# Performance work log

Hardware: AMD Instinct MI355X
Metric: run time of the kernel (lower is better)

## Reference

```python
import jax, jax.numpy as jnp
import numpy as np

B, C, H, W = 16, 1, 512, 512
D, F, KH, KW = 4, 24, 5, 5   # numWienerFilters, output_features, reg-filter size
BKH, BKW = 9, 9              # blur kernel size
LB, UB = 1e-4, 1e-2


def psf2otf(psf, shape):
    # zero-pad psf to `shape`, circularly shift its center to (0,0), FFT
    kh, kw = psf.shape[-2], psf.shape[-1]
    pad = [(0, 0)] * (psf.ndim - 2) + [(0, shape[0] - kh), (0, shape[1] - kw)]
    p = jnp.pad(psf, pad)
    p = jnp.roll(p, shift=(-((kh - 1) // 2), -((kw - 1) // 2)), axis=(-2, -1))
    return jnp.fft.fft2(p)


def _taper_profile(proj, n):
    # autocorrelation of the psf projection, periodized to length n (MATLAB edgetaper)
    z = jnp.zeros(n - 1, proj.dtype).at[: proj.shape[0]].set(proj)
    zf = jnp.fft.fft(z)
    acf = jnp.real(jnp.fft.ifft(zf * jnp.conj(zf)))
    acf = jnp.concatenate([acf, acf[:1]])
    return acf / acf.max()


def _normalize_weights(w, scale):
    # WeightNormalization5D: zero-mean + L2-normalize over (C,kh,kw), times scale
    w = w - w.mean(axis=(2, 3, 4), keepdims=True)
    nrm = jnp.sqrt(jnp.sum(w * w, axis=(2, 3, 4), keepdims=True))
    return w * (scale[..., None, None, None] / nrm)


def setup_inputs():
    key = jax.random.key(0)
    ks = jax.random.split(key, 4)
    x = jax.random.uniform(ks[0], (B, C, H, W), jnp.float32)
    bk = jax.random.uniform(ks[1], (BKH, BKW), jnp.float32) + 1e-3
    bk = bk / bk.sum()  # normalized blur PSF
    stdn = jax.random.uniform(ks[2], (B,), jnp.float32) * 0.1 + 0.01
    conv_weights = jax.random.normal(ks[3], (D, F, C, KH, KW), jnp.float32)
    scale = jnp.full((D, F), 0.1, jnp.float32)
    alpha = jnp.log(jnp.logspace(np.log10(LB), np.log10(UB), D))[:, None].astype(jnp.float32)
    return {"x": x, "blur_kernel": bk, "stdn": stdn,
            "conv_weights": conv_weights, "scale": scale, "alpha": alpha}


def reference(x, blur_kernel, stdn, conv_weights, scale, alpha):
    kh, kw = blur_kernel.shape
    # getPad2RetainShape
    pt, pb = (kh + 1) // 2 - 1, kh - (kh + 1) // 2
    pl, pr = (kw + 1) // 2 - 1, kw - (kw + 1) // 2
    xp = jnp.pad(x, ((0, 0), (0, 0), (pt, pb), (pl, pr)), mode="symmetric")
    Hp, Wp = xp.shape[-2], xp.shape[-1]
    otf = psf2otf(blur_kernel, (Hp, Wp))                     # (Hp,Wp) complex
    # EdgeTaper: blend image with its circular blur near borders
    br = _taper_profile(blur_kernel.sum(axis=1), Hp)
    bc = _taper_profile(blur_kernel.sum(axis=0), Wp)
    taper = (1.0 - br)[:, None] * (1.0 - bc)[None, :]
    blurred = jnp.real(jnp.fft.ifft2(jnp.fft.fft2(xp) * otf))
    xp = taper * xp + (1.0 - taper) * blurred
    # regularization-filter OTFs
    w = _normalize_weights(conv_weights, scale)              # (D,F,C,kh,kw)
    G = psf2otf(w, (Hp, Wp))                                 # (D,F,C,Hp,Wp)
    S = jnp.sum(G.real ** 2 + G.imag ** 2, axis=1)           # (D,C,Hp,Wp)
    a = jnp.exp(alpha)[:, :, None, None]                     # (D,1,1,1)
    B2 = otf.real ** 2 + otf.imag ** 2                       # (Hp,Wp)
    denom = B2[None, None] + a * S                           # (D,C,Hp,Wp)
    Y = jnp.conj(otf) * jnp.fft.fft2(xp)                     # (B,C,Hp,Wp)
    Xf = Y[:, None] / denom[None]                            # (B,D,C,Hp,Wp)
    out = jnp.real(jnp.fft.ifft2(Xf))[..., pt:Hp - pb, pl:Wp - pr]
    # colored-noise std factor per (wiener filter, channel)
    cvar = jnp.mean(B2[None, None] / denom ** 2, axis=(-2, -1))   # (D,C)
    cvar = jnp.broadcast_to(cvar[None], (x.shape[0],) + cvar.shape)  # (B,D,C)
    cstdn = jnp.sqrt(stdn[:, None] ** 2 * cvar.mean(axis=2))        # (B,D)
    return out, cstdn
```

## Files before the change

kernel.cpp:

```cpp
#include <hip/hip_runtime.h>
#include <math.h>

#define NP    520
#define NN    (520*520)
#define HH    512
#define NPIX  (512*512)
#define NB    16
#define NPAIR 8
#define ND    4
#define NF    24
#define KS    544
#define RS    576
#define PLANE ((size_t)RS*KS)
#define S8P   (8*PLANE)
#define E9SZ  (NP*9)
#define CSZ   (ND*9*NP)
#define NBORD 18396
#define PADCH 5536
#define NBLK2 1057
#define TWO_PI 6.283185307179586f

typedef unsigned short u16;
typedef __attribute__((ext_vector_type(8))) short bf16x8;
typedef __attribute__((ext_vector_type(4))) float f32x4;

__device__ __forceinline__ int wrap520(int t){ t %= NP; return t < 0 ? t + NP : t; }

__device__ __forceinline__ u16 f2bf(float f){
  unsigned u = __float_as_uint(f);
  u += 0x7FFFu + ((u >> 16) & 1u);
  return (u16)(u >> 16);
}
__device__ __forceinline__ float bf2f(u16 h){
  return __uint_as_float(((unsigned)h) << 16);
}
__device__ __forceinline__ void gll16(const u16* g, u16* l){
  __builtin_amdgcn_global_load_lds(
      (const __attribute__((address_space(1))) void*)g,
      (__attribute__((address_space(3))) void*)l, 16, 0, 0);
}
template<int N> __device__ __forceinline__ void vmwait(){
  if constexpr (N == 0)       asm volatile("s_waitcnt vmcnt(0)" ::: "memory");
  else if constexpr (N == 4)  asm volatile("s_waitcnt vmcnt(4)" ::: "memory");
  else if constexpr (N == 6)  asm volatile("s_waitcnt vmcnt(6)" ::: "memory");
  else if constexpr (N == 8)  asm volatile("s_waitcnt vmcnt(8)" ::: "memory");
  else if constexpr (N == 12) asm volatile("s_waitcnt vmcnt(12)" ::: "memory");
}
#define MF(a,b,c) __builtin_amdgcn_mfma_f32_16x16x32_bf16((a),(b),(c),0,0,0)


__global__ __launch_bounds__(256) void zwb_k(u16* __restrict__ slabs,
                                             u16* __restrict__ wf, u16* __restrict__ wi){
  int idx = blockIdx.x*256 + threadIdx.x;
  const int nA = 16*PADCH;
  if (idx < nA){
    int pl = idx / PADCH, cc = idx % PADCH;
    int row, col;
    if (cc < 1728){ row = cc/3; col = 520 + (cc%3)*8; }
    else { int c2 = cc - 1728; row = 520 + c2/68; col = (c2%68)*8; }
    bf16x8 z = {0,0,0,0,0,0,0,0};
    *(bf16x8*)(slabs + (size_t)pl*PLANE + (size_t)row*KS + col) = z;
    return;
  }
  idx -= nA;
  if (idx >= (int)PLANE) return;
  int r = idx / KS, k = idx % KS;
  float fr=0.f, fi=0.f, ir=0.f, ii=0.f;
  if (r < NP && k < NP){
    int m = (int)(((long long)r * (long long)k) % NP);
    float ang = TWO_PI * (float)m / (float)NP;
    float s, c; sincosf(ang, &s, &c);
    fr = c; fi = -s;
    ir = c * (1.0f/NP); ii = s * (1.0f/NP);
  }
  wf[0*PLANE+idx] = f2bf(fr); wf[1*PLANE+idx] = f2bf(fi);
  wi[0*PLANE+idx] = f2bf(ir); wi[1*PLANE+idx] = f2bf(ii);
}

__global__ __launch_bounds__(256) void setup1_k(const float* __restrict__ bk,
                                                const float* __restrict__ cw,
                                                const float* __restrict__ scale,
                                                float* __restrict__ e9,
                                                float* __restrict__ r_row, float* __restrict__ r_col,
                                                float* __restrict__ wn){
  int idx = blockIdx.x*256 + threadIdx.x;
  if (idx < NP*9){
    int u = idx / 9, t = idx % 9;
    int m = wrap520(u*(t-4));
    float ang = TWO_PI * (float)m / (float)NP;
    float s, c; sincosf(ang, &s, &c);
    e9[idx] = c; e9[E9SZ + idx] = -s;
    return;
  }
  idx -= NP*9;
  if (idx < 18){
    int k = idx % 9;
    bool rowp = (idx < 9);
    float proj[9];
    for (int m = 0; m < 9; ++m){
      float a = 0.f;
      for (int j = 0; j < 9; ++j) a += rowp ? bk[m*9+j] : bk[j*9+m];
      proj[m] = a;
    }
    float acc = 0.f;
    for (int m = 0; m + k < 9; ++m) acc += proj[m] * proj[m+k];
    (rowp ? r_row : r_col)[k] = acc;
    return;
  }
  idx -= 18;
  if (idx >= ND*NF) return;
  const float* wp = cw + idx*25;
  float mean = 0.f;
  for (int k = 0; k < 25; ++k) mean += wp[k];
  mean *= (1.0f/25.0f);
  float ss = 0.f;
  for (int k = 0; k < 25; ++k){ float d = wp[k]-mean; ss += d*d; }
  float sc = scale[idx] / sqrtf(ss);
  for (int k = 0; k < 25; ++k) wn[idx*25+k] = (wp[k]-mean)*sc;
}

__global__ __launch_bounds__(256) void setup2_k(const float* __restrict__ bk,
                                                const float* __restrict__ e9,
                                                const float* __restrict__ wn,
                                                float* __restrict__ T, float* __restrict__ R){
  int idx = blockIdx.x*256 + threadIdx.x;
  if (idx < 9*NP){
    int i = idx / NP, v = idx % NP;
    float tr = 0.f, ti = 0.f;
    #pragma unroll
    for (int j = 0; j < 9; ++j){
      float w = bk[i*9+j];
      tr += w * e9[v*9+j];
      ti += w * e9[E9SZ + v*9+j];
    }
    T[idx] = tr; T[9*NP + idx] = ti;
    return;
  }
  idx -= 9*NP;
  if (idx >= ND*81) return;
  int d = idx / 81, t = idx % 81;
  int di = t/9 - 4, dj = t%9 - 4;
  int i0 = di > 0 ? di : 0, i1 = di < 0 ? 4+di : 4;
  int j0 = dj > 0 ? dj : 0, j1 = dj < 0 ? 4+dj : 4;
  float acc = 0.f;
  for (int f = 0; f < NF; ++f){
    const float* w = wn + (d*NF+f)*25;
    for (int i = i0; i <= i1; ++i)
      for (int j = j0; j <= j1; ++j)
        acc += w[i*5+j] * w[(i-di)*5 + (j-dj)];
  }
  R[idx] = acc;
}

__global__ void C_k(const float* __restrict__ R, const float* __restrict__ e9,
                    float* __restrict__ Ctab){
  int idx = blockIdx.x*blockDim.x + threadIdx.x;
  if (idx >= ND*9*NP) return;
  int v = idx % NP, t9 = idx / NP;
  int d = t9 / 9, t = t9 % 9;
  float cr = 0.f, ci = 0.f;
  #pragma unroll
  for (int s = 0; s < 9; ++s){
    float r = R[d*81 + t*9 + s];
    cr += r * e9[v*9+s];
    ci += r * e9[E9SZ + v*9+s];
  }
  Ctab[idx] = cr; Ctab[CSZ + idx] = ci;
}

__global__ __launch_bounds__(256) void denomMT2_k(
    const float* __restrict__ Tb, const float* __restrict__ e9,
    const float* __restrict__ Ctab, const float* __restrict__ alpha,
    u16* __restrict__ MTre, u16* __restrict__ MTim, float* __restrict__ pcv){
  __shared__ float e9r[2304], e9i[2304];
  __shared__ float red[256];
  const int tid = threadIdx.x;
  const int p = blockIdx.x*256 + tid;
  {
    int u0 = (blockIdx.x*256) % NP;
    for (int i = tid; i < 2304; i += 256){
      int row = i / 9, col = i % 9;
      int uu = u0 + row; if (uu >= NP) uu -= NP;
      e9r[i] = e9[uu*9 + col];
      e9i[i] = e9[E9SZ + uu*9 + col];
    }
  }
  __syncthreads();
  float contrib[ND] = {0.f, 0.f, 0.f, 0.f};
  if (p < NN){
    int v = p / NP;
    float er9[9], ei9[9];
    #pragma unroll
    for (int i = 0; i < 9; ++i){ er9[i] = e9r[tid*9+i]; ei9[i] = e9i[tid*9+i]; }
    float ar = 0.f, ai = 0.f;
    #pragma unroll
    for (int i = 0; i < 9; ++i){
      float tr = Tb[i*NP+v], ti = Tb[9*NP + i*NP+v];
      ar += er9[i]*tr - ei9[i]*ti;
      ai += er9[i]*ti + ei9[i]*tr;
    }
    float B2 = ar*ar + ai*ai;
    #pragma unroll
    for (int d = 0; d < ND; ++d){
      float S = 0.f;
      #pragma unroll
      for (int t = 0; t < 9; ++t)
        S += er9[t]*Ctab[(d*9+t)*NP + v] - ei9[t]*Ctab[CSZ + (d*9+t)*NP + v];
      float dv = B2 + expf(alpha[d]) * S;
      MTre[(size_t)d*NN + p] = f2bf(ar / dv);
      MTim[(size_t)d*NN + p] = f2bf(-ai / dv);
      contrib[d] = B2 / (dv*dv);
    }
  }
  for (int d = 0; d < ND; ++d){
    red[tid] = contrib[d]; __syncthreads();
    for (int s = 128; s > 0; s >>= 1){
      if (tid < s) red[tid] += red[tid+s];
      __syncthreads();
    }
    if (tid == 0) pcv[(size_t)blockIdx.x*ND + d] = red[0];
    __syncthreads();
  }
}

__global__ __launch_bounds__(256) void cstdn2_k(const float* __restrict__ stdn,
                                                const float* __restrict__ pcv,
                                                float* __restrict__ out){
  __shared__ float red[256];
  int t = threadIdx.x;
  int d = t & 3, ch = t >> 2;
  float acc = 0.f;
  for (int b = ch; b < NBLK2; b += 64) acc += pcv[(size_t)b*ND + d];
  red[t] = acc; __syncthreads();
  for (int s = 128; s >= 4; s >>= 1){
    if (t < s) red[t] += red[t+s];
    __syncthreads();
  }
  if (t < NB*ND){
    int b = t >> 2, d2 = t & 3;
    float s = stdn[b];
    out[(size_t)NB*ND*NPIX + t] = sqrtf(s*s*red[d2]*(1.0f/(float)NN));
  }
}

__global__ __launch_bounds__(256) void pad_tr_k(const float* __restrict__ x,
                                                u16* __restrict__ MA){
  __shared__ float tile[64][65];
  const int q  = blockIdx.z;
  const int r0 = blockIdx.y * 64;
  const int c0 = blockIdx.x * 64;
  const int t  = threadIdx.x;
  const float* xq = x + (size_t)q*NPIX;
  const int jl = t & 63, ib = t >> 6;
  const bool fast = (c0 >= 64 && c0 <= 448 && r0 >= 64 && r0 <= 448);

  if (fast){
    #pragma unroll 1
    for (int pass = 0; pass < 16; ++pass){
      int il = ib + pass*4;
      tile[il][jl] = xq[(size_t)(c0+il-4)*HH + (r0+jl-4)];
    }
  } else {
    #pragma unroll 1
    for (int pass = 0; pass < 16; ++pass){
      int il = ib + pass*4;
      int I = c0 + il, J = r0 + jl;
      float v = 0.f;
      if (I < NP && J < NP){
        int si = I - 4; si = (si < 0) ? (-si-1) : ((si >= HH) ? (2*HH-1-si) : si);
        int sj = J - 4; sj = (sj < 0) ? (-sj-1) : ((sj >= HH) ? (2*HH-1-sj) : sj);
        v = xq[(size_t)si*HH + sj];
      }
      tile[il][jl] = v;
    }
  }
  __syncthreads();

  const int cchunk = t & 7, rb = t >> 3;
  const int pair = q >> 1, pl = q & 1;
  #pragma unroll
  for (int half = 0; half < 2; ++half){
    int rl = rb + half*32;
    int r = r0 + rl, cg = c0 + cchunk*8;
    if (r >= NP || cg >= NP) continue;
    bf16x8 vh;
    #pragma unroll
    for (int e = 0; e < 8; ++e)
      vh[e] = (short)f2bf(tile[cchunk*8+e][rl]);
    size_t o = (size_t)pair*PLANE + (size_t)r*KS + cg;
    *(bf16x8*)(MA + (size_t)pl*S8P + o) = vh;
  }
}

__global__ __launch_bounds__(256) void border_k(const float* __restrict__ x,
                                                const float* __restrict__ bk,
                                                const float* __restrict__ r_row,
                                                const float* __restrict__ r_col,
                                                u16* __restrict__ MA){
  __shared__ float bks[81], rr_[9], rc_[9];
  if (threadIdx.x < 81) bks[threadIdx.x] = bk[threadIdx.x];
  if (threadIdx.x < 9){ rr_[threadIdx.x] = r_row[threadIdx.x]; rc_[threadIdx.x] = r_col[threadIdx.x]; }
  __syncthreads();
  int idx = blockIdx.x*256 + threadIdx.x;
  if (idx >= NB*NBORD) return;
  int q = idx / NBORD, t = idx % NBORD;
  int I, J;
  if (t < 9360){ int ri = t / 520; I = (ri < 9) ? ri : 502 + ri; J = t % 520; }
  else { int s = t - 9360; I = 9 + s / 18; int ci = s % 18; J = (ci < 9) ? ci : 502 + ci; }
  const float* xq = x + (size_t)q*NPIX;
  auto XP = [&](int ii, int jj)->float{
    int si = ii - 4; si = (si < 0) ? (-si-1) : ((si >= HH) ? (2*HH-1-si) : si);
    int sj = jj - 4; sj = (sj < 0) ? (-sj-1) : ((sj >= HH) ? (2*HH-1-sj) : sj);
    return xq[(size_t)si*HH + sj];
  };
  float v = XP(I, J);
  float brv = (I < 9) ? rr_[I] : ((I >= 511) ? rr_[519-I] : 0.f);
  float bcv = (J < 9) ? rc_[J] : ((J >= 511) ? rc_[519-J] : 0.f);
  brv /= rr_[0]; bcv /= rc_[0];
  float tp = (1.f - brv) * (1.f - bcv);
  float blur = 0.f;
  for (int a = 0; a < 9; ++a){
    int ii = wrap520(I - a + 4);
    for (int b2 = 0; b2 < 9; ++b2){
      int jj = wrap520(J - b2 + 4);
      blur += bks[a*9+b2] * XP(ii, jj);
    }
  }
  v = tp*v + (1.f - tp)*blur;
  int pair = q >> 1, pl = q & 1;
  MA[(size_t)pl*S8P + (size_t)pair*PLANE + (size_t)J*KS + I] = f2bf(v);
}

__global__ __launch_bounds__(256) void maskF_k(const u16* __restrict__ IN, u16* __restrict__ OUT,
                                               const u16* __restrict__ Mre, const u16* __restrict__ Mim){
  int idx = blockIdx.x*256 + threadIdx.x;
  if (idx >= NPAIR*NP*65) return;
  int pr = idx / (NP*65), rem = idx % (NP*65);
  int r = rem / 65, c0 = (rem % 65)*8;
  size_t o = (size_t)pr*PLANE + (size_t)r*KS + c0;
  bf16x8 qr = *(const bf16x8*)(IN + 0*S8P + o);
  bf16x8 qi = *(const bf16x8*)(IN + 1*S8P + o);
  const u16* mrp = Mre + (size_t)r*NP + c0;
  const u16* mip = Mim + (size_t)r*NP + c0;
  bf16x8 o0, o1;
  #pragma unroll
  for (int e = 0; e < 8; ++e){
    float vr = bf2f((u16)qr[e]), vi = bf2f((u16)qi[e]);
    float mr = bf2f(mrp[e]), mi = bf2f(mip[e]);
    o0[e] = (short)f2bf(vr*mr - vi*mi);
    o1[e] = (short)f2bf(vr*mi + vi*mr);
  }
  *(bf16x8*)(OUT + 0*S8P + o) = o0;
  *(bf16x8*)(OUT + 1*S8P + o) = o1;
}

template<int BM, int CROP, int MASKOUT>
__global__ __launch_bounds__(256) void gemm_k(
    const u16* __restrict__ P, size_t pPl, size_t pZp, size_t pZd,
    const u16* __restrict__ Q, size_t qPl, size_t qZp, size_t qZd,
    u16* __restrict__ O, size_t oPl, size_t oZp, size_t oZd,
    float* __restrict__ cropOut, int dBase,
    const u16* __restrict__ Mre, const u16* __restrict__ Mim)
{
  constexpr int NW = 4;
  constexpr int FR = BM/32;
  constexpr int TR = BM/16;
  constexpr int LPW = 4*TR/NW;
  constexpr int PLSTR = BM*32;
  constexpr int BUF = 4*PLSTR;
  constexpr int NK = KS/32;
  __shared__ u16 lds[3*BUF];
  const int tid = threadIdx.x;
  const int l = tid & 63, w = tid >> 6;

  const int gx = gridDim.x, gy = gridDim.y;
  int lin = blockIdx.x + gx*(blockIdx.y + gy*blockIdx.z);
  int ntot = gx*gy*gridDim.z;
  int q8 = ntot >> 3, r8 = ntot & 7;
  int xcd = lin & 7, id8 = lin >> 3;
  int nl = (xcd < r8 ? xcd*(q8+1) : r8*(q8+1) + (xcd-r8)*q8) + id8;
  int BX = nl % gx; int t2 = nl / gx;
  int BY = t2 % gy; int BZ = t2 / gy;

  const int pair = BZ & 7;
  const int dd = dBase + (BZ >> 3);
  const int R0 = BY * BM, C0 = BX * BM;

  const u16* Pb = P + (size_t)pair*pZp + (size_t)dd*pZd;
  const u16* Qb = Q + (size_t)pair*qZp + (size_t)dd*qZd;

  const int s = l >> 2;
  const int cs8 = ((l & 3) ^ ((s >> 1) & 3)) * 8;
  const size_t pOff0 = (size_t)(R0 + s)*KS + cs8;
  const size_t qOff0 = (size_t)(C0 + s)*KS + cs8;

  const int lm = l & 15, lc = l >> 4;
  const int wm = w >> 1, wn = w & 1;

  f32x4 zero4 = {0.f, 0.f, 0.f, 0.f};
  f32x4 aRe[FR][FR], aIm[FR][FR];
  #pragma unroll
  for (int i = 0; i < FR; ++i)
    #pragma unroll
    for (int j = 0; j < FR; ++j){ aRe[i][j] = zero4; aIm[i][j] = zero4; }

  auto STAGE = [&](int bi, int k0){
    u16* dst = lds + bi*BUF;
    #pragma unroll
    for (int i = 0; i < LPW; ++i){
      int t = w + i*NW;
      int q2 = t / TR, r2 = t % TR;
      const u16* src = (q2 < 2) ? (Pb + (size_t)q2*pPl + pOff0)
                                : (Qb + (size_t)(q2-2)*qPl + qOff0);
      gll16(src + (size_t)(r2*16)*KS + k0, dst + q2*PLSTR + r2*512);
    }
  };

  STAGE(0, 0);
  STAGE(1, 32);

  #pragma unroll 1
  for (int kt = 0; kt < NK; ++kt){
    if (kt + 1 < NK) vmwait<LPW>(); else vmwait<0>();
    __builtin_amdgcn_sched_barrier(0);
    __builtin_amdgcn_s_barrier();
    __builtin_amdgcn_sched_barrier(0);

    const u16* buf = lds + (kt%3)*BUF;
    bf16x8 pf[FR][2];
    #pragma unroll
    for (int mi = 0; mi < FR; ++mi){
      int r = wm*(FR*16) + mi*16 + lm;
      int co = ((lc ^ ((r >> 1) & 3)) << 3);
      pf[mi][0] = *(const bf16x8*)(buf + 0*PLSTR + r*32 + co);
      pf[mi][1] = *(const bf16x8*)(buf + 1*PLSTR + r*32 + co);
    }
    #pragma unroll
    for (int ni = 0; ni < FR; ++ni){
      int rq = wn*(FR*16) + ni*16 + lm;
      int cq = ((lc ^ ((rq >> 1) & 3)) << 3);
      bf16x8 q0 = *(const bf16x8*)(buf + 2*PLSTR + rq*32 + cq);
      bf16x8 q1 = *(const bf16x8*)(buf + 3*PLSTR + rq*32 + cq);
      if (ni == 0){
        if (kt + 2 < NK) STAGE((kt+2)%3, (kt+2)*32);
      } else {
        __builtin_amdgcn_sched_barrier(0);
        __builtin_amdgcn_s_barrier();
      }
      asm volatile("s_waitcnt lgkmcnt(0)" ::: "memory");
      __builtin_amdgcn_sched_barrier(0);
      __builtin_amdgcn_s_setprio(1);
      #pragma unroll
      for (int mi = 0; mi < FR; ++mi){
        bf16x8 nw = pf[mi][1] ^ (short)0x8000;
        f32x4 re = aRe[mi][ni], im = aIm[mi][ni];
        re = MF(pf[mi][0], q0, re);
        re = MF(nw,        q1, re);
        im = MF(pf[mi][0], q1, im);
        im = MF(pf[mi][1], q0, im);
        aRe[mi][ni] = re; aIm[mi][ni] = im;
      }
      __builtin_amdgcn_s_setprio(0);
    }
  }

  u16* Ob = O ? (O + (size_t)pair*oZp + (size_t)dd*oZd) : nullptr;
  #pragma unroll
  for (int mi = 0; mi < FR; ++mi)
    #pragma unroll
    for (int ni = 0; ni < FR; ++ni){
      int cb = C0 + wn*(FR*16) + ni*16 + lm;
      int rb = R0 + wm*(FR*16) + mi*16 + lc*4;
      #pragma unroll
      for (int e = 0; e < 4; ++e){
        int rr = rb + e;
        float vr = aRe[mi][ni][e], vi = aIm[mi][ni][e];
        if (CROP){
          if (rr >= 4 && rr < 516 && cb >= 4 && cb < 516){
            size_t px = (size_t)(rr-4)*HH + (cb-4);
            cropOut[((size_t)(2*pair  )*ND + dd)*NPIX + px] = vr;
            cropOut[((size_t)(2*pair+1)*ND + dd)*NPIX + px] = vi;
          }
        } else if (MASKOUT){
          if (cb < KS){
            size_t o = (size_t)rr*KS + cb;
            size_t mo = (size_t)(rr < NP ? rr : 0)*NP + (cb < NP ? cb : 0);
            #pragma unroll
            for (int d2 = 0; d2 < ND; ++d2){
              float mr = bf2f(Mre[(size_t)d2*NN + mo]);
              float mi2 = bf2f(Mim[(size_t)d2*NN + mo]);
              u16* Od = O + (size_t)d2*oZd + (size_t)pair*oZp;
              Od[0*oPl+o] = f2bf(vr*mr - vi*mi2);
              Od[1*oPl+o] = f2bf(vr*mi2 + vi*mr);
            }
          }
        } else {
          if (cb < KS){
            size_t o = (size_t)rr*KS + cb;
            Ob[0*oPl+o] = f2bf(vr);
            Ob[1*oPl+o] = f2bf(vi);
          }
        }
      }
    }
}


extern "C" void kernel_launch(void* const* d_in, const int* in_sizes, int n_in,
                              void* d_out, int out_size, void* d_ws, size_t ws_size,
                              hipStream_t stream){
  const float* x     = (const float*)d_in[0];
  const float* bk    = (const float*)d_in[1];
  const float* stdn  = (const float*)d_in[2];
  const float* cw    = (const float*)d_in[3];
  const float* scale = (const float*)d_in[4];
  const float* alpha = (const float*)d_in[5];
  float* out = (float*)d_out;

  char* base = (char*)d_ws;
  const size_t UNIT = 16*PLANE*sizeof(u16);
  size_t off;
  auto alloc = [&](size_t bytes)->void*{
    void* p = base + off;
    off += (bytes + 255) & ~(size_t)255;
    return p;
  };

  u16 *MA, *MB, *MC, *Dm, *Do, *WF, *WI, *MTre, *MTim;
  float *e9, *Tb, *Rarr, *Ctab, *r_row, *r_col, *wn, *pcv;
  auto layout = [&](bool bigL){
    off = 0;
    MA = (u16*)alloc(UNIT);
    MB = (u16*)alloc(UNIT);
    if (bigL){ Dm = (u16*)alloc(4*UNIT); Do = (u16*)alloc(4*UNIT); MC = nullptr; }
    else     { MC = (u16*)alloc(UNIT);   Dm = nullptr; Do = nullptr; }
    WF = (u16*)alloc(2*PLANE*sizeof(u16));
    WI = (u16*)alloc(2*PLANE*sizeof(u16));
    MTre = (u16*)alloc((size_t)ND*NN*2);
    MTim = (u16*)alloc((size_t)ND*NN*2);
    e9   = (float*)alloc(2*E9SZ*4);
    Tb   = (float*)alloc(2*9*NP*4);
    Rarr = (float*)alloc(ND*81*4);
    Ctab = (float*)alloc(2*CSZ*4);
    r_row = (float*)alloc(64);
    r_col = (float*)alloc(64);
    wn   = (float*)alloc(ND*NF*25*4);
    pcv  = (float*)alloc((size_t)NBLK2*ND*4);
    return off;
  };
  bool big = (layout(true) <= ws_size);
  if (!big){
    if (layout(false) > ws_size) return;
  }

  {
    int ztot = 16*PADCH + (int)PLANE;
    zwb_k<<<(ztot+255)/256, 256, 0, stream>>>(MA, WF, WI);
  }
  setup1_k<<<(NP*9+18+ND*NF+255)/256, 256, 0, stream>>>(bk, cw, scale, e9, r_row, r_col, wn);
  setup2_k<<<(9*NP+ND*81+255)/256, 256, 0, stream>>>(bk, e9, wn, Tb, Rarr);
  C_k     <<<(ND*9*NP+255)/256, 256, 0, stream>>>(Rarr, e9, Ctab);
  denomMT2_k<<<NBLK2, 256, 0, stream>>>(Tb, e9, Ctab, alpha, MTre, MTim, pcv);
  cstdn2_k<<<1, 256, 0, stream>>>(stdn, pcv, out);
  pad_tr_k<<<dim3(9, 9, NB), 256, 0, stream>>>(x, MA);
  border_k<<<(NB*NBORD+255)/256, 256, 0, stream>>>(x, bk, r_row, r_col, MA);

  gemm_k<64,0,0><<<dim3(9,9,8),256,0,stream>>>(
      WF, PLANE, 0, 0,   MA, S8P, PLANE, 0,   MB, S8P, PLANE, 0,
      nullptr, 0, nullptr, nullptr);

  if (big){
    gemm_k<64,0,1><<<dim3(9,9,8),256,0,stream>>>(
        WF, PLANE, 0, 0,   MB, S8P, PLANE, 0,   Dm, S8P, PLANE, 16*PLANE,
        nullptr, 0, MTre, MTim);
    gemm_k<96,0,0><<<dim3(6,6,32),256,0,stream>>>(
        WI, PLANE, 0, 0,   Dm, S8P, PLANE, 16*PLANE,   Do, S8P, PLANE, 16*PLANE,
        nullptr, 0, nullptr, nullptr);
    gemm_k<96,1,0><<<dim3(6,6,32),256,0,stream>>>(
        Do, S8P, PLANE, 16*PLANE,   WI, PLANE, 0, 0,   nullptr, 0, 0, 0,
        out, 0, nullptr, nullptr);
  } else {
    gemm_k<64,0,0><<<dim3(9,9,8),256,0,stream>>>(
        WF, PLANE, 0, 0,   MB, S8P, PLANE, 0,   MC, S8P, PLANE, 0,
        nullptr, 0, nullptr, nullptr);
    const int mgrid = (NPAIR*NP*65 + 255)/256;
    for (int d = 0; d < ND; ++d){
      maskF_k<<<mgrid,256,0,stream>>>(MC, MA, MTre + (size_t)d*NN, MTim + (size_t)d*NN);
      gemm_k<96,0,0><<<dim3(6,6,8),256,0,stream>>>(
          WI, PLANE, 0, 0,   MA, S8P, PLANE, 0,   MB, S8P, PLANE, 0,
          nullptr, 0, nullptr, nullptr);
      gemm_k<96,1,0><<<dim3(6,6,8),256,0,stream>>>(
          MB, S8P, PLANE, 0,   WI, PLANE, 0, 0,   nullptr, 0, 0, 0,
          out, d, nullptr, nullptr);
    }
  }
}
```

Measured before the change: 275.2 us.

## Stage GEMM epilogue through LDS for vectorized stores; cache denom tables in LDS

```diff
diff --git a/kernel.cpp b/kernel.cpp
--- a/kernel.cpp
+++ b/kernel.cpp
@@ -173,29 +173,43 @@
     const float* __restrict__ Ctab, const float* __restrict__ alpha,
     u16* __restrict__ MTre, u16* __restrict__ MTim, float* __restrict__ pcv){
   __shared__ float e9r[2304], e9i[2304];
-  __shared__ float red[256];
+  __shared__ float tbs[2][2][9];
+  __shared__ float cts[2][2][36];
+  __shared__ f32x4 red[256];
   const int tid = threadIdx.x;
-  const int p = blockIdx.x*256 + tid;
+  const int p0 = blockIdx.x*256;
+  const int p = p0 + tid;
+  const int v0 = p0 / NP;
   {
-    int u0 = (blockIdx.x*256) % NP;
+    int u0 = p0 % NP;
     for (int i = tid; i < 2304; i += 256){
       int row = i / 9, col = i % 9;
       int uu = u0 + row; if (uu >= NP) uu -= NP;
       e9r[i] = e9[uu*9 + col];
       e9i[i] = e9[E9SZ + uu*9 + col];
     }
+    if (tid < 36){
+      int s = tid / 18, rem = tid % 18, h = rem / 9, i = rem % 9;
+      int vv = v0 + s; if (vv >= NP) vv = NP-1;
+      tbs[s][h][i] = Tb[h*(9*NP) + i*NP + vv];
+    } else if (tid < 36 + 144){
+      int t = tid - 36;
+      int s = t / 72, rem = t % 72, h = rem / 36, j = rem % 36;
+      int vv = v0 + s; if (vv >= NP) vv = NP-1;
+      cts[s][h][j] = Ctab[(size_t)h*CSZ + (size_t)j*NP + vv];
+    }
   }
   __syncthreads();
-  float contrib[ND] = {0.f, 0.f, 0.f, 0.f};
+  f32x4 contrib = {0.f, 0.f, 0.f, 0.f};
   if (p < NN){
-    int v = p / NP;
+    int sl = p/NP - v0;
     float er9[9], ei9[9];
     #pragma unroll
     for (int i = 0; i < 9; ++i){ er9[i] = e9r[tid*9+i]; ei9[i] = e9i[tid*9+i]; }
     float ar = 0.f, ai = 0.f;
     #pragma unroll
     for (int i = 0; i < 9; ++i){
-      float tr = Tb[i*NP+v], ti = Tb[9*NP + i*NP+v];
+      float tr = tbs[sl][0][i], ti = tbs[sl][1][i];
       ar += er9[i]*tr - ei9[i]*ti;
       ai += er9[i]*ti + ei9[i]*tr;
     }
@@ -205,22 +219,19 @@
       float S = 0.f;
       #pragma unroll
       for (int t = 0; t < 9; ++t)
-        S += er9[t]*Ctab[(d*9+t)*NP + v] - ei9[t]*Ctab[CSZ + (d*9+t)*NP + v];
+        S += er9[t]*cts[sl][0][d*9+t] - ei9[t]*cts[sl][1][d*9+t];
       float dv = B2 + expf(alpha[d]) * S;
       MTre[(size_t)d*NN + p] = f2bf(ar / dv);
       MTim[(size_t)d*NN + p] = f2bf(-ai / dv);
       contrib[d] = B2 / (dv*dv);
     }
   }
-  for (int d = 0; d < ND; ++d){
-    red[tid] = contrib[d]; __syncthreads();
-    for (int s = 128; s > 0; s >>= 1){
-      if (tid < s) red[tid] += red[tid+s];
-      __syncthreads();
-    }
-    if (tid == 0) pcv[(size_t)blockIdx.x*ND + d] = red[0];
+  red[tid] = contrib; __syncthreads();
+  for (int s = 128; s > 0; s >>= 1){
+    if (tid < s) red[tid] += red[tid+s];
     __syncthreads();
   }
+  if (tid < ND) pcv[(size_t)blockIdx.x*ND + tid] = red[0][tid];
 }
 
 __global__ __launch_bounds__(256) void cstdn2_k(const float* __restrict__ stdn,
@@ -369,6 +380,7 @@
   constexpr int PLSTR = BM*32;
   constexpr int BUF = 4*PLSTR;
   constexpr int NK = KS/32;
+  constexpr int WC = FR*16;
   __shared__ u16 lds[3*BUF];
   const int tid = threadIdx.x;
   const int l = tid & 63, w = tid >> 6;
@@ -430,14 +442,14 @@
     bf16x8 pf[FR][2];
     #pragma unroll
     for (int mi = 0; mi < FR; ++mi){
-      int r = wm*(FR*16) + mi*16 + lm;
+      int r = wm*WC + mi*16 + lm;
       int co = ((lc ^ ((r >> 1) & 3)) << 3);
       pf[mi][0] = *(const bf16x8*)(buf + 0*PLSTR + r*32 + co);
       pf[mi][1] = *(const bf16x8*)(buf + 1*PLSTR + r*32 + co);
     }
     #pragma unroll
     for (int ni = 0; ni < FR; ++ni){
-      int rq = wn*(FR*16) + ni*16 + lm;
+      int rq = wn*WC + ni*16 + lm;
       int cq = ((lc ^ ((rq >> 1) & 3)) << 3);
       bf16x8 q0 = *(const bf16x8*)(buf + 2*PLSTR + rq*32 + cq);
       bf16x8 q1 = *(const bf16x8*)(buf + 3*PLSTR + rq*32 + cq);
@@ -464,45 +476,110 @@
     }
   }
 
-  u16* Ob = O ? (O + (size_t)pair*oZp + (size_t)dd*oZd) : nullptr;
-  #pragma unroll
-  for (int mi = 0; mi < FR; ++mi)
-    #pragma unroll
-    for (int ni = 0; ni < FR; ++ni){
-      int cb = C0 + wn*(FR*16) + ni*16 + lm;
-      int rb = R0 + wm*(FR*16) + mi*16 + lc*4;
+  const int r0w = R0 + wm*WC;
+  const int c0w = C0 + wn*WC;
+
+  if (CROP){
+    float* cp = cropOut;
+    #pragma unroll
+    for (int mi = 0; mi < FR; ++mi)
       #pragma unroll
-      for (int e = 0; e < 4; ++e){
-        int rr = rb + e;
-        float vr = aRe[mi][ni][e], vi = aIm[mi][ni][e];
-        if (CROP){
+      for (int ni = 0; ni < FR; ++ni){
+        int cb = c0w + ni*16 + lm;
+        int rb = r0w + mi*16 + lc*4;
+        #pragma unroll
+        for (int e = 0; e < 4; ++e){
+          int rr = rb + e;
           if (rr >= 4 && rr < 516 && cb >= 4 && cb < 516){
             size_t px = (size_t)(rr-4)*HH + (cb-4);
-            cropOut[((size_t)(2*pair  )*ND + dd)*NPIX + px] = vr;
-            cropOut[((size_t)(2*pair+1)*ND + dd)*NPIX + px] = vi;
-          }
-        } else if (MASKOUT){
-          if (cb < KS){
-            size_t o = (size_t)rr*KS + cb;
-            size_t mo = (size_t)(rr < NP ? rr : 0)*NP + (cb < NP ? cb : 0);
-            #pragma unroll
-            for (int d2 = 0; d2 < ND; ++d2){
-              float mr = bf2f(Mre[(size_t)d2*NN + mo]);
-              float mi2 = bf2f(Mim[(size_t)d2*NN + mo]);
-              u16* Od = O + (size_t)d2*oZd + (size_t)pair*oZp;
-              Od[0*oPl+o] = f2bf(vr*mr - vi*mi2);
-              Od[1*oPl+o] = f2bf(vr*mi2 + vi*mr);
-            }
-          }
-        } else {
-          if (cb < KS){
-            size_t o = (size_t)rr*KS + cb;
-            Ob[0*oPl+o] = f2bf(vr);
-            Ob[1*oPl+o] = f2bf(vi);
+            cp[((size_t)(2*pair  )*ND + dd)*NPIX + px] = aRe[mi][ni][e];
+            cp[((size_t)(2*pair+1)*ND + dd)*NPIX + px] = aIm[mi][ni][e];
           }
         }
       }
-    }
+    return;
+  }
+
+  __builtin_amdgcn_sched_barrier(0);
+  __builtin_amdgcn_s_barrier();
+  __builtin_amdgcn_sched_barrier(0);
+  u16* st = lds + w*(2*16*WC);
+  constexpr int VR = WC/8;
+
+  if (MASKOUT){
+    #pragma unroll 1
+    for (int d2 = 0; d2 < ND; ++d2){
+      u16* Od = O + (size_t)d2*oZd + (size_t)pair*oZp;
+      const u16* MreD = Mre + (size_t)d2*NN;
+      const u16* MimD = Mim + (size_t)d2*NN;
+      #pragma unroll 1
+      for (int mi = 0; mi < FR; ++mi){
+        #pragma unroll
+        for (int ni = 0; ni < FR; ++ni){
+          int cb = c0w + ni*16 + lm;
+          #pragma unroll
+          for (int e = 0; e < 4; ++e){
+            int rr = r0w + mi*16 + lc*4 + e;
+            size_t mo = (size_t)(rr < NP ? rr : 0)*NP + (cb < NP ? cb : 0);
+            float mr = bf2f(MreD[mo]), mi2 = bf2f(MimD[mo]);
+            float vr = aRe[mi][ni][e], vi = aIm[mi][ni][e];
+            st[0*16*WC + (lc*4+e)*WC + ni*16+lm] = f2bf(vr*mr - vi*mi2);
+            st[1*16*WC + (lc*4+e)*WC + ni*16+lm] = f2bf(vr*mi2 + vi*mr);
+          }
+        }
+        asm volatile("s_waitcnt lgkmcnt(0)" ::: "memory");
+        __builtin_amdgcn_sched_barrier(0);
+        #pragma unroll
+        for (int i0 = 0; i0 < 16*VR; i0 += 64){
+          int i = i0 + l;
+          if (i < 16*VR){
+            int row = i / VR, vec = i % VR;
+            int gr = r0w + mi*16 + row;
+            int gc = c0w + vec*8;
+            if (gc < KS){
+              bf16x8 v0 = *(bf16x8*)(st + 0*16*WC + row*WC + vec*8);
+              bf16x8 v1 = *(bf16x8*)(st + 1*16*WC + row*WC + vec*8);
+              *(bf16x8*)(Od + 0*oPl + (size_t)gr*KS + gc) = v0;
+              *(bf16x8*)(Od + 1*oPl + (size_t)gr*KS + gc) = v1;
+            }
+          }
+        }
+        asm volatile("s_waitcnt lgkmcnt(0)" ::: "memory");
+        __builtin_amdgcn_sched_barrier(0);
+      }
+    }
+  } else {
+    u16* Ob = O + (size_t)pair*oZp + (size_t)dd*oZd;
+    #pragma unroll 1
+    for (int mi = 0; mi < FR; ++mi){
+      #pragma unroll
+      for (int ni = 0; ni < FR; ++ni)
+        #pragma unroll
+        for (int e = 0; e < 4; ++e){
+          st[0*16*WC + (lc*4+e)*WC + ni*16+lm] = f2bf(aRe[mi][ni][e]);
+          st[1*16*WC + (lc*4+e)*WC + ni*16+lm] = f2bf(aIm[mi][ni][e]);
+        }
+      asm volatile("s_waitcnt lgkmcnt(0)" ::: "memory");
+      __builtin_amdgcn_sched_barrier(0);
+      #pragma unroll
+      for (int i0 = 0; i0 < 16*VR; i0 += 64){
+        int i = i0 + l;
+        if (i < 16*VR){
+          int row = i / VR, vec = i % VR;
+          int gr = r0w + mi*16 + row;
+          int gc = c0w + vec*8;
+          if (gc < KS){
+            bf16x8 v0 = *(bf16x8*)(st + 0*16*WC + row*WC + vec*8);
+            bf16x8 v1 = *(bf16x8*)(st + 1*16*WC + row*WC + vec*8);
+            *(bf16x8*)(Ob + 0*oPl + (size_t)gr*KS + gc) = v0;
+            *(bf16x8*)(Ob + 1*oPl + (size_t)gr*KS + gc) = v1;
+          }
+        }
+      }
+      asm volatile("s_waitcnt lgkmcnt(0)" ::: "memory");
+      __builtin_amdgcn_sched_barrier(0);
+    }
+  }
 }
 
 
```

New measurement: 315.6 us. +14.7%, slower.
